# Kernel tuning notes

Measured on AMD Instinct MI355X. Metric: run time of the kernel, lower is better.

## Reference

```python
import jax, jax.numpy as jnp
import numpy as np
import math

# dims
B, L, D = 2, 2048, 1024          # batch, seq len, embedding_dim
HID, ATT, H = 1024, 512, 8       # linear_hidden_dim, attention_dim, num_heads
DQK, DUV = ATT // H, HID // H    # 64, 128
NBUCK = 64                       # time_num_buckets
MAX_SPAN = 86400 * 90            # max_time_span
EPS = 1e-6
OUT_DIM = 2 * HID + 2 * ATT      # uvqk output dim = 3072


def _time_boundaries():
    # RelativeAttentionBiasModule._build_boundaries: pure log buckets
    steps = NBUCK - 1
    log_part = np.exp(np.linspace(0.0, math.log(MAX_SPAN), steps))
    b = np.unique(np.floor(np.clip(log_part, 1, None)).astype(np.int64)).astype(np.float32)
    return jnp.asarray(b)

_BOUNDARIES = _time_boundaries()  # len <= 63, indices < NBUCK


def setup_inputs() -> dict:
    key = jax.random.key(0)
    ks = jax.random.split(key, 8)
    x = jax.random.normal(ks[0], (B, L, D), dtype=jnp.float32)
    timestamps = jnp.sort(
        jax.random.randint(ks[1], (B, L), 0, 2592000), axis=-1
    )  # chronological event times (seconds)
    attn_mask = jnp.tril(jnp.ones((L, L), dtype=bool))[None].repeat(B, axis=0)  # causal
    W_uvqk = jax.random.normal(ks[2], (OUT_DIM, D), dtype=jnp.float32) * 0.02
    b_uvqk = jnp.zeros((OUT_DIM,), dtype=jnp.float32)
    time_bias = jax.random.normal(ks[3], (NBUCK, H), dtype=jnp.float32) * 0.02
    W_o = jax.random.normal(ks[4], (D, HID), dtype=jnp.float32) * 0.02
    b_o = jnp.zeros((D,), dtype=jnp.float32)
    rms_w = jnp.ones((HID,), dtype=jnp.float32)
    return {"x": x, "timestamps": timestamps, "attn_mask": attn_mask,
            "W_uvqk": W_uvqk, "b_uvqk": b_uvqk, "time_bias": time_bias,
            "W_o": W_o, "b_o": b_o, "rms_w": rms_w}


def reference(x, timestamps, attn_mask, W_uvqk, b_uvqk, time_bias, W_o, b_o, rms_w):
    Bx, Lx, _ = x.shape
    scale = 1.0 / math.sqrt(DQK)

    # fused uvqk projection + act1 (silu)
    h = jax.nn.silu(x @ W_uvqk.T + b_uvqk)  # [B, L, OUT_DIM]
    u, v, q, k = jnp.split(h, [HID, 2 * HID, 2 * HID + ATT], axis=-1)

    def heads(t, d):  # [B, L, H*d] -> [B, H, L, d]
        return t.reshape(Bx, Lx, H, d).transpose(0, 2, 1, 3)

    u = heads(u, DUV)
    v = heads(v, DUV)
    q = heads(q, DQK) * scale
    k = heads(k, DQK)

    logits = jnp.einsum('bhid,bhjd->bhij', q.astype(jnp.float32), k.astype(jnp.float32))

    # bucketized relative-time bias (per-head)
    tdiff = jnp.abs(timestamps[:, :, None] - timestamps[:, None, :])
    tdiff = jnp.clip(tdiff, 1, None).astype(jnp.float32)  # clamp_min(1)
    bk = jnp.searchsorted(_BOUNDARIES, tdiff, side='left')  # torch.bucketize right=False
    rab = time_bias[bk].transpose(0, 3, 1, 2)  # [B, H, L, L]

    # pointwise silu attention (no softmax), masked
    A = jax.nn.silu(logits + rab) * attn_mask[:, None].astype(jnp.float32)

    y = jnp.einsum('bhij,bhjd->bhid', A, v)               # [B, H, L, DUV]
    y = y.transpose(0, 2, 1, 3).reshape(Bx, Lx, HID)       # merge heads
    u_m = u.transpose(0, 2, 1, 3).reshape(Bx, Lx, HID)

    # RMSNorm then U-gate
    rms = y * jax.lax.rsqrt(jnp.mean(y * y, axis=-1, keepdims=True) + EPS) * rms_w
    y_point = rms.astype(x.dtype) * u_m

    return y_point @ W_o.T + b_o  # [B, L, D]
```

## Files before the change

kernel.cpp:

```cpp
#include <hip/hip_runtime.h>
#include <hip/hip_bf16.h>

typedef float f32x4 __attribute__((ext_vector_type(4)));
typedef short s16x8 __attribute__((ext_vector_type(8)));
typedef short s16x4 __attribute__((ext_vector_type(4)));
typedef unsigned short u16x4 __attribute__((ext_vector_type(4)));

__device__ __forceinline__ float bf2f(unsigned short u) {
    union { unsigned int i; float f; } x; x.i = ((unsigned int)u) << 16; return x.f;
}
__device__ __forceinline__ unsigned short f2bf(float f) {
    union { float f; unsigned int i; } x; x.f = f;
    unsigned int r = x.i + 0x7FFFu + ((x.i >> 16) & 1u);
    return (unsigned short)(r >> 16);
}
__device__ __forceinline__ float silu(float v) {
    return v / (1.f + __expf(-v));
}
__device__ __forceinline__ float silu_fast(float v) {
    return v * __builtin_amdgcn_rcpf(1.f + __expf(-v));
}

#define GLDS16(gp, lp) __builtin_amdgcn_global_load_lds( \
    (const __attribute__((address_space(1))) unsigned int*)(gp), \
    (__attribute__((address_space(3))) unsigned int*)(lp), 16, 0, 0)

__global__ __launch_bounds__(256) void cvt_bf16(
    const float* __restrict__ X, const float* __restrict__ W,
    const float* __restrict__ Wo,
    unsigned short* __restrict__ Xb, unsigned short* __restrict__ Wb,
    unsigned short* __restrict__ Wob)
{
    int idx = blockIdx.x * 256 + threadIdx.x;
    const float* src; unsigned short* dst; int off;
    if (idx < 1048576)       { src = X;  dst = Xb;  off = idx; }
    else if (idx < 1835008)  { src = W;  dst = Wb;  off = idx - 1048576; }
    else                     { src = Wo; dst = Wob; off = idx - 1835008; }
    f32x4 v = *reinterpret_cast<const f32x4*>(&src[(size_t)off * 4]);
    u16x4 o;
    #pragma unroll
    for (int j = 0; j < 4; ++j) o[j] = f2bf(v[j]);
    *reinterpret_cast<u16x4*>(&dst[(size_t)off * 4]) = o;
}

__global__ __launch_bounds__(256) void bucketize(
    const int* __restrict__ TS, unsigned char* __restrict__ BK)
{
    const int jt = blockIdx.x, it = blockIdx.y, b = blockIdx.z;
    if (jt > it) return;
    __shared__ int bndRaw[63];
    __shared__ int bnd[64];
    __shared__ int tsi[64], tsj[64];
    const int tid = threadIdx.x;
    if (tid < 63) {
        double step = log(7776000.0) / 62.0;
        double v = exp(step * (double)tid);
        if (v < 1.0) v = 1.0;
        bndRaw[tid] = (int)floor(v);
    }
    if (tid >= 64 && tid < 128) tsi[tid - 64] = TS[b * 2048 + it * 64 + (tid - 64)];
    else if (tid >= 128 && tid < 192) tsj[tid - 128] = TS[b * 2048 + jt * 64 + (tid - 128)];
    __syncthreads();
    if (tid == 0) {
        int c = 0, p = -1;
        for (int i = 0; i < 63; ++i) { int x = bndRaw[i]; if (x != p) { bnd[c++] = x; p = x; } }
        for (; c < 64; ++c) bnd[c] = 0x7FFFFFFF;
    }
    __syncthreads();
    const int il = tid & 63, jc = (tid >> 6) * 16;
    const int tiv = tsi[il];
    unsigned char out[16];
    #pragma unroll
    for (int u = 0; u < 16; ++u) {
        int td = tiv - tsj[jc + u]; td = td < 0 ? -td : td; if (td < 1) td = 1;
        int pos = 0;
        #pragma unroll
        for (int st = 32; st; st >>= 1)
            if (bnd[pos + st - 1] < td) pos += st;
        out[u] = (unsigned char)pos;
    }
    *reinterpret_cast<int4*>(&BK[((size_t)b << 22) + (size_t)(it * 64 + il) * 2048 + jt * 64 + jc]) =
        *reinterpret_cast<const int4*>(out);
}

__global__ __launch_bounds__(256) void gemm_uvqk(
    const unsigned short* __restrict__ Xb, const unsigned short* __restrict__ Wb,
    const float* __restrict__ bias,
    unsigned short* __restrict__ U, unsigned short* __restrict__ Vt,
    unsigned short* __restrict__ Q, unsigned short* __restrict__ K)
{
    __shared__ __align__(16) unsigned short smem[2][128][64];
    const int tid = threadIdx.x;
    const int wv = tid >> 6, lane = tid & 63;
    const int g = lane >> 4, lr = lane & 15;
    const int wid = (blockIdx.x & 7) * 96 + (blockIdx.x >> 3);
    const int m0 = (wid & 31) * 128, n0 = (wid >> 5) * 128;
    const int wr = (wv >> 1) * 64, wc = (wv & 1) * 64;
    const int ls = lr & 7;
    f32x4 acc[4][4] = {};

    for (int k0 = 0; k0 < 1024; k0 += 64) {
        #pragma unroll
        for (int c = 0; c < 4; ++c) {
            int id = c * 256 + tid;
            int row = id >> 3, c8 = id & 7;
            int sc = (c8 ^ (row & 7)) * 8;
            GLDS16(&Xb[(size_t)(m0 + row) * 1024 + k0 + sc], &smem[0][row][c8 * 8]);
            GLDS16(&Wb[(size_t)(n0 + row) * 1024 + k0 + sc], &smem[1][row][c8 * 8]);
        }
        __syncthreads();
        s16x8 afr[4][2], bfr[4][2];
        #pragma unroll
        for (int i = 0; i < 4; ++i)
            #pragma unroll
            for (int kq = 0; kq < 2; ++kq) {
                afr[i][kq] = *reinterpret_cast<const s16x8*>(
                    &smem[0][wr + i * 16 + lr][((kq * 4 + g) ^ ls) * 8]);
                bfr[i][kq] = *reinterpret_cast<const s16x8*>(
                    &smem[1][wc + i * 16 + lr][((kq * 4 + g) ^ ls) * 8]);
            }
        #pragma unroll
        for (int kq = 0; kq < 2; ++kq)
            #pragma unroll
            for (int mi = 0; mi < 4; ++mi)
                #pragma unroll
                for (int ni = 0; ni < 4; ++ni)
                    acc[mi][ni] = __builtin_amdgcn_mfma_f32_16x16x32_bf16(
                        afr[mi][kq], bfr[ni][kq], acc[mi][ni], 0, 0, 0);
        __syncthreads();
    }

    if (n0 >= 1024 && n0 < 2048) {
        const int head = (n0 - 1024) >> 7;
        unsigned short* sT = &smem[0][0][0] + wv * (32 * 72);
        #pragma unroll
        for (int hh = 0; hh < 2; ++hh) {
            #pragma unroll
            for (int nn = 0; nn < 2; ++nn) {
                int ni = hh * 2 + nn;
                float bn = bias[n0 + wc + ni * 16 + lr];
                #pragma unroll
                for (int mi = 0; mi < 4; ++mi)
                    #pragma unroll
                    for (int r = 0; r < 4; ++r)
                        sT[(nn * 16 + lr) * 72 + mi * 16 + g * 4 + r] =
                            f2bf(silu(acc[mi][ni][r] + bn));
            }
            #pragma unroll
            for (int c = 0; c < 4; ++c) {
                int id = c * 64 + lane;
                int row = id >> 3, ch = id & 7;
                s16x8 val = *reinterpret_cast<const s16x8*>(&sT[row * 72 + ch * 8]);
                int d = wc + hh * 32 + row;
                int mg = m0 + wr + ch * 8;
                int bb = mg >> 11, l = mg & 2047;
                *reinterpret_cast<s16x8*>(
                    &Vt[(((size_t)(bb * 8 + head) * 128 + d) << 11) + l]) = val;
            }
        }
    } else {
        #pragma unroll
        for (int ni = 0; ni < 4; ++ni) {
            int n = n0 + wc + ni * 16 + lr;
            float bn = bias[n];
            #pragma unroll
            for (int mi = 0; mi < 4; ++mi) {
                #pragma unroll
                for (int r = 0; r < 4; ++r) {
                    int m = m0 + wr + mi * 16 + g * 4 + r;
                    float v = silu(acc[mi][ni][r] + bn);
                    int b = m >> 11, l = m & 2047;
                    if (n < 1024) {
                        U[(size_t)m * 1024 + n] = f2bf(v);
                    } else if (n < 2560) {
                        int dd = n - 2048, h = dd >> 6, d = dd & 63;
                        Q[((((size_t)(b * 8 + h) << 11) + l) << 6) + d] = f2bf(v * 0.125f);
                    } else {
                        int dd = n - 2560, h = dd >> 6, d = dd & 63;
                        K[((((size_t)(b * 8 + h) << 11) + l) << 6) + d] = f2bf(v);
                    }
                }
            }
        }
    }
}

__global__ __launch_bounds__(512, 1) void attn(
    const unsigned short* __restrict__ Q, const unsigned short* __restrict__ K,
    const unsigned short* __restrict__ Vt, const unsigned char* __restrict__ BK,
    const float* __restrict__ TB, float* __restrict__ Y)
{
    __shared__ __align__(16) unsigned short sK[2][2][64][64];
    __shared__ __align__(16) unsigned short sV[2][2][128][64];
    __shared__ __align__(16) unsigned char  sBK[2][2][64][64];

    const int tid = threadIdx.x, wv = tid >> 6, lane = tid & 63;
    const int g = lane >> 4, lr = lane & 15;

    const int bid = blockIdx.x;
    const int xcd = bid & 7, kix = bid >> 3;
    const int bh = 2 * xcd + (kix & 1);
    const int ti = 31 - (kix >> 1);
    const int b = bh >> 3, h = bh & 7;
    const int i0 = ti * 64;
    const int rg = wv & 3;
    const int half = wv >> 2;
    const int irow = i0 + rg * 16;
    const int P = (ti + 2) >> 1;

    const int tbl = __float_as_int(TB[lane * 8 + h]);

    const unsigned short* qb = Q + ((size_t)bh << 11) * 64;
    const unsigned short* kb = K + ((size_t)bh << 11) * 64;
    const unsigned short* vtb = Vt + ((size_t)bh << 7) * 2048;
    const unsigned char* bkb = BK + ((size_t)b << 22);

    s16x8 aq[2];
    #pragma unroll
    for (int kq = 0; kq < 2; ++kq)
        aq[kq] = *reinterpret_cast<const s16x8*>(&qb[(size_t)(irow + lr) * 64 + kq * 32 + g * 8]);

    char* sKb = (char*)&sK[0][0][0][0];
    char* sVb = (char*)&sV[0][0][0][0];
    char* sBKb = (char*)&sBK[0][0][0][0];
    const int cs = lr & 7;
    const int ib = irow + lr;

    auto stage = [&](int q, int db) {
        int jth = 2 * q + half;
        if (jth > ti) jth = 2 * q;
        const size_t j0 = (size_t)jth * 64;
        char* kd = sKb + db * 16384 + half * 8192;
        char* vd = sVb + db * 32768 + half * 16384;
        char* bkd = sBKb + db * 8192 + half * 4096;
        #pragma unroll
        for (int c = 0; c < 2; ++c) {
            int chunk = rg * 128 + c * 64 + lane;
            int row = chunk >> 3, c8 = chunk & 7;
            GLDS16(kb + (j0 + row) * 64 + ((c8 ^ (row & 7)) * 8), kd + chunk * 16);
        }
        #pragma unroll
        for (int c = 0; c < 4; ++c) {
            int chunk = rg * 256 + c * 64 + lane;
            int d = chunk >> 3, c8 = chunk & 7;
            GLDS16(vtb + (size_t)d * 2048 + j0 + ((c8 ^ (d & 7)) * 8), vd + chunk * 16);
        }
        {
            int chunk = rg * 64 + lane;
            int row = chunk >> 2, c16 = chunk & 3;
            GLDS16(bkb + (size_t)(i0 + row) * 2048 + j0 + ((c16 ^ (row & 3)) * 16), bkd + chunk * 16);
        }
    };

    f32x4 accy[8] = {};

#define COMPUTE(DB) { \
        const int jt = 2 * p + half; \
        if (jt <= ti) { \
            const char* kbase = sKb + (DB) * 16384 + half * 8192; \
            f32x4 sacc[4] = {}; \
            _Pragma("unroll") \
            for (int ni = 0; ni < 4; ++ni) { \
                _Pragma("unroll") \
                for (int kq = 0; kq < 2; ++kq) { \
                    s16x8 kf = *reinterpret_cast<const s16x8*>( \
                        kbase + (ni * 16 + lr) * 128 + (((kq * 4 + g) ^ cs) << 4)); \
                    sacc[ni] = __builtin_amdgcn_mfma_f32_16x16x32_bf16(kf, aq[kq], sacc[ni], 0, 0, 0); \
                } \
            } \
            const int j0 = jt * 64; \
            const bool diag = (jt == ti); \
            s16x4 pf[4]; \
            _Pragma("unroll") \
            for (int ni = 0; ni < 4; ++ni) { \
                unsigned int bw = *reinterpret_cast<const unsigned int*>( \
                    sBKb + (DB) * 8192 + half * 4096 + (rg * 16 + lr) * 64 + ((ni ^ (lr & 3)) << 4) + g * 4); \
                float b0 = __int_as_float(__builtin_amdgcn_ds_bpermute((int)((bw & 255u) << 2), tbl)); \
                float b1 = __int_as_float(__builtin_amdgcn_ds_bpermute((int)(((bw >> 8) & 255u) << 2), tbl)); \
                float b2 = __int_as_float(__builtin_amdgcn_ds_bpermute((int)(((bw >> 16) & 255u) << 2), tbl)); \
                float b3 = __int_as_float(__builtin_amdgcn_ds_bpermute((int)((bw >> 24) << 2), tbl)); \
                float v0 = silu_fast(sacc[ni][0] + b0); \
                float v1 = silu_fast(sacc[ni][1] + b1); \
                float v2 = silu_fast(sacc[ni][2] + b2); \
                float v3 = silu_fast(sacc[ni][3] + b3); \
                if (diag) { \
                    int jb = j0 + ni * 16 + g * 4; \
                    if (jb + 0 > ib) v0 = 0.f; \
                    if (jb + 1 > ib) v1 = 0.f; \
                    if (jb + 2 > ib) v2 = 0.f; \
                    if (jb + 3 > ib) v3 = 0.f; \
                } \
                unsigned int w0, w1; \
                asm("v_cvt_pk_bf16_f32 %0, %1, %2" : "=v"(w0) : "v"(v0), "v"(v1)); \
                asm("v_cvt_pk_bf16_f32 %0, %1, %2" : "=v"(w1) : "v"(v2), "v"(v3)); \
                union { unsigned int u_[2]; s16x4 v_; } cvt_; \
                cvt_.u_[0] = w0; cvt_.u_[1] = w1; \
                pf[ni] = cvt_.v_; \
            } \
            const char* vbase = sVb + (DB) * 32768 + half * 16384; \
            _Pragma("unroll") \
            for (int di = 0; di < 8; ++di) { \
                _Pragma("unroll") \
                for (int ni = 0; ni < 4; ++ni) { \
                    s16x4 vf = *reinterpret_cast<const s16x4*>( \
                        vbase + (di * 16 + lr) * 128 + (((2 * ni + (g >> 1)) ^ cs) << 4) + ((g & 1) << 3)); \
                    accy[di] = __builtin_amdgcn_mfma_f32_16x16x16bf16_1k(pf[ni], vf, accy[di], 0, 0, 0); \
                } \
            } \
        } }

    stage(0, 0);

    int p = 0;
    for (;;) {
        __builtin_amdgcn_s_barrier();
        if (p + 1 < P) {
            stage(p + 1, 1);
            asm volatile("s_waitcnt vmcnt(7)" ::: "memory");
        } else {
            asm volatile("s_waitcnt vmcnt(0)" ::: "memory");
        }
        __builtin_amdgcn_s_barrier();
        COMPUTE(0);
        if (++p == P) break;
        __builtin_amdgcn_s_barrier();
        if (p + 1 < P) {
            stage(p + 1, 0);
            asm volatile("s_waitcnt vmcnt(7)" ::: "memory");
        } else {
            asm volatile("s_waitcnt vmcnt(0)" ::: "memory");
        }
        __builtin_amdgcn_s_barrier();
        COMPUTE(1);
        if (++p == P) break;
    }
#undef COMPUTE

    __syncthreads();
    float* red = (float*)sVb;
    if (wv >= 4) {
        #pragma unroll
        for (int di = 0; di < 8; ++di)
            #pragma unroll
            for (int r = 0; r < 4; ++r)
                red[(rg * 16 + g * 4 + r) * 132 + di * 16 + lr] = accy[di][r];
    }
    __syncthreads();
    if (wv < 4) {
        #pragma unroll
        for (int di = 0; di < 8; ++di)
            #pragma unroll
            for (int r = 0; r < 4; ++r) {
                float s = accy[di][r] + red[(rg * 16 + g * 4 + r) * 132 + di * 16 + lr];
                Y[(size_t)((b << 11) + irow + g * 4 + r) * 1024 + h * 128 + di * 16 + lr] = s;
            }
    }
}

__global__ __launch_bounds__(256) void rmsnorm_gate(
    const float* __restrict__ Y, const unsigned short* __restrict__ U,
    const float* __restrict__ rw, unsigned short* __restrict__ YP)
{
    __shared__ float red[4];
    const int row = blockIdx.x, tid = threadIdx.x;
    f32x4 v = *reinterpret_cast<const f32x4*>(&Y[(size_t)row * 1024 + tid * 4]);
    float ss = v[0] * v[0] + v[1] * v[1] + v[2] * v[2] + v[3] * v[3];
    #pragma unroll
    for (int off = 32; off; off >>= 1) ss += __shfl_down(ss, off);
    if ((tid & 63) == 0) red[tid >> 6] = ss;
    __syncthreads();
    float rms = rsqrtf((red[0] + red[1] + red[2] + red[3]) * (1.f / 1024.f) + 1e-6f);
    #pragma unroll
    for (int j = 0; j < 4; ++j) {
        int c = tid * 4 + j;
        float o = v[j] * rms * rw[c] * bf2f(U[(size_t)row * 1024 + c]);
        YP[(size_t)row * 1024 + c] = f2bf(o);
    }
}

__global__ __launch_bounds__(512) void gemm_out(
    const unsigned short* __restrict__ YP, const unsigned short* __restrict__ Wob,
    const float* __restrict__ bo, float* __restrict__ OUT)
{
    __shared__ __align__(16) unsigned short sA[128][64];
    __shared__ __align__(16) unsigned short sB[128][64];
    const int tid = threadIdx.x;
    const int wv = tid >> 6, lane = tid & 63;
    const int g = lane >> 4, lr = lane & 15;
    const int wid = (blockIdx.x & 7) * 32 + (blockIdx.x >> 3);
    const int m0 = (wid & 31) * 128, n0 = (wid >> 5) * 128;
    const int wr = (wv >> 2) * 64, wc = (wv & 3) * 32;
    const int ls = lr & 7;
    f32x4 acc[4][2] = {};

    for (int k0 = 0; k0 < 1024; k0 += 64) {
        #pragma unroll
        for (int c = 0; c < 2; ++c) {
            int id = c * 512 + tid;
            int row = id >> 3, c8 = id & 7;
            int sc = (c8 ^ (row & 7)) * 8;
            GLDS16(&YP[(size_t)(m0 + row) * 1024 + k0 + sc], &sA[row][c8 * 8]);
            GLDS16(&Wob[(size_t)(n0 + row) * 1024 + k0 + sc], &sB[row][c8 * 8]);
        }
        __syncthreads();
        s16x8 afr[4][2], bfr[2][2];
        #pragma unroll
        for (int kq = 0; kq < 2; ++kq) {
            #pragma unroll
            for (int i = 0; i < 4; ++i)
                afr[i][kq] = *reinterpret_cast<const s16x8*>(
                    &sA[wr + i * 16 + lr][((kq * 4 + g) ^ ls) * 8]);
            #pragma unroll
            for (int i = 0; i < 2; ++i)
                bfr[i][kq] = *reinterpret_cast<const s16x8*>(
                    &sB[wc + i * 16 + lr][((kq * 4 + g) ^ ls) * 8]);
        }
        #pragma unroll
        for (int kq = 0; kq < 2; ++kq)
            #pragma unroll
            for (int mi = 0; mi < 4; ++mi)
                #pragma unroll
                for (int ni = 0; ni < 2; ++ni)
                    acc[mi][ni] = __builtin_amdgcn_mfma_f32_16x16x32_bf16(
                        afr[mi][kq], bfr[ni][kq], acc[mi][ni], 0, 0, 0);
        __syncthreads();
    }

    #pragma unroll
    for (int ni = 0; ni < 2; ++ni) {
        int n = n0 + wc + ni * 16 + lr;
        float bn = bo[n];
        #pragma unroll
        for (int mi = 0; mi < 4; ++mi)
            #pragma unroll
            for (int r = 0; r < 4; ++r) {
                int m = m0 + wr + mi * 16 + g * 4 + r;
                OUT[(size_t)m * 1024 + n] = acc[mi][ni][r] + bn;
            }
    }
}

extern "C" void kernel_launch(void* const* d_in, const int* in_sizes, int n_in,
                              void* d_out, int out_size, void* d_ws, size_t ws_size,
                              hipStream_t stream) {
    const float* X     = (const float*)d_in[0];
    const int*   TS    = (const int*)d_in[1];
    const float* Wuvqk = (const float*)d_in[3];
    const float* buvqk = (const float*)d_in[4];
    const float* TB    = (const float*)d_in[5];
    const float* Wo    = (const float*)d_in[6];
    const float* bo    = (const float*)d_in[7];
    const float* rw    = (const float*)d_in[8];
    float* OUT = (float*)d_out;

    char* ws = (char*)d_ws;
    unsigned short* Qb  = (unsigned short*)(ws);
    unsigned short* Kb  = (unsigned short*)(ws + (4u << 20));
    unsigned short* Vt  = (unsigned short*)(ws + (8u << 20));
    unsigned short* Ub  = (unsigned short*)(ws + (16u << 20));
    float*          Yb  = (float*)(ws + (24u << 20));
    unsigned short* Xb  = (unsigned short*)(ws + (24u << 20));
    unsigned short* Wb  = (unsigned short*)(ws + (32u << 20));
    unsigned short* YP  = (unsigned short*)(ws + (40u << 20));
    unsigned char*  BKm = (unsigned char*)(ws + (48u << 20));
    unsigned short* Wob = (unsigned short*)(ws + (56u << 20));

    cvt_bf16<<<8192, 256, 0, stream>>>(X, Wuvqk, Wo, Xb, Wb, Wob);
    bucketize<<<dim3(32, 32, 2), 256, 0, stream>>>(TS, BKm);
    gemm_uvqk<<<768, 256, 0, stream>>>(Xb, Wb, buvqk, Ub, Vt, Qb, Kb);
    attn<<<512, 512, 0, stream>>>(Qb, Kb, Vt, BKm, TB, Yb);
    rmsnorm_gate<<<4096, 256, 0, stream>>>(Yb, Ub, rw, YP);
    gemm_out<<<256, 512, 0, stream>>>(YP, Wob, bo, OUT);
}
```

Before: 149.7 us.

## Merge convert and bucketize kernels, store attention output in bf16, tweak GEMM loops

Fuses the bf16 conversion and time-bucketize kernels into one launch to remove a kernel launch. Stores the attention output as bf16 instead of fp32, which halves the traffic into the RMSNorm kernel at the cost of some precision before normalization. Also switches the SiLU epilogue to a reciprocal-based fast variant and restructures the GEMM inner loops to load fragments per k-step, which reduces register pressure.

New measurement: 144.6 us. 3.4% less time.

```diff
diff --git a/kernel.cpp b/kernel.cpp
--- a/kernel.cpp
+++ b/kernel.cpp
@@ -14,9 +14,6 @@
     unsigned int r = x.i + 0x7FFFu + ((x.i >> 16) & 1u);
     return (unsigned short)(r >> 16);
 }
-__device__ __forceinline__ float silu(float v) {
-    return v / (1.f + __expf(-v));
-}
 __device__ __forceinline__ float silu_fast(float v) {
     return v * __builtin_amdgcn_rcpf(1.f + __expf(-v));
 }
@@ -25,33 +22,32 @@
     (const __attribute__((address_space(1))) unsigned int*)(gp), \
     (__attribute__((address_space(3))) unsigned int*)(lp), 16, 0, 0)
 
-__global__ __launch_bounds__(256) void cvt_bf16(
+__global__ __launch_bounds__(256) void cvt_bucketize(
     const float* __restrict__ X, const float* __restrict__ W,
-    const float* __restrict__ Wo,
+    const float* __restrict__ Wo, const int* __restrict__ TS,
     unsigned short* __restrict__ Xb, unsigned short* __restrict__ Wb,
-    unsigned short* __restrict__ Wob)
+    unsigned short* __restrict__ Wob, unsigned char* __restrict__ BK)
 {
-    int idx = blockIdx.x * 256 + threadIdx.x;
-    const float* src; unsigned short* dst; int off;
-    if (idx < 1048576)       { src = X;  dst = Xb;  off = idx; }
-    else if (idx < 1835008)  { src = W;  dst = Wb;  off = idx - 1048576; }
-    else                     { src = Wo; dst = Wob; off = idx - 1835008; }
-    f32x4 v = *reinterpret_cast<const f32x4*>(&src[(size_t)off * 4]);
-    u16x4 o;
-    #pragma unroll
-    for (int j = 0; j < 4; ++j) o[j] = f2bf(v[j]);
-    *reinterpret_cast<u16x4*>(&dst[(size_t)off * 4]) = o;
-}
-
-__global__ __launch_bounds__(256) void bucketize(
-    const int* __restrict__ TS, unsigned char* __restrict__ BK)
-{
-    const int jt = blockIdx.x, it = blockIdx.y, b = blockIdx.z;
+    const int tid = threadIdx.x;
+    if (blockIdx.x < 8192) {
+        int idx = blockIdx.x * 256 + tid;
+        const float* src; unsigned short* dst; int off;
+        if (idx < 1048576)       { src = X;  dst = Xb;  off = idx; }
+        else if (idx < 1835008)  { src = W;  dst = Wb;  off = idx - 1048576; }
+        else                     { src = Wo; dst = Wob; off = idx - 1835008; }
+        f32x4 v = *reinterpret_cast<const f32x4*>(&src[(size_t)off * 4]);
+        u16x4 o;
+        #pragma unroll
+        for (int j = 0; j < 4; ++j) o[j] = f2bf(v[j]);
+        *reinterpret_cast<u16x4*>(&dst[(size_t)off * 4]) = o;
+        return;
+    }
+    const int bid = blockIdx.x - 8192;
+    const int jt = bid & 31, it = (bid >> 5) & 31, b = bid >> 10;
     if (jt > it) return;
     __shared__ int bndRaw[63];
     __shared__ int bnd[64];
     __shared__ int tsi[64], tsj[64];
-    const int tid = threadIdx.x;
     if (tid < 63) {
         double step = log(7776000.0) / 62.0;
         double v = exp(step * (double)tid);
@@ -89,7 +85,8 @@
     unsigned short* __restrict__ U, unsigned short* __restrict__ Vt,
     unsigned short* __restrict__ Q, unsigned short* __restrict__ K)
 {
-    __shared__ __align__(16) unsigned short smem[2][128][64];
+    __shared__ __align__(16) unsigned short sA[128][64];
+    __shared__ __align__(16) unsigned short sB[128][64];
     const int tid = threadIdx.x;
     const int wv = tid >> 6, lane = tid & 63;
     const int g = lane >> 4, lr = lane & 15;
@@ -105,34 +102,33 @@
             int id = c * 256 + tid;
             int row = id >> 3, c8 = id & 7;
             int sc = (c8 ^ (row & 7)) * 8;
-            GLDS16(&Xb[(size_t)(m0 + row) * 1024 + k0 + sc], &smem[0][row][c8 * 8]);
-            GLDS16(&Wb[(size_t)(n0 + row) * 1024 + k0 + sc], &smem[1][row][c8 * 8]);
+            GLDS16(&Xb[(size_t)(m0 + row) * 1024 + k0 + sc], &sA[row][c8 * 8]);
+            GLDS16(&Wb[(size_t)(n0 + row) * 1024 + k0 + sc], &sB[row][c8 * 8]);
         }
         __syncthreads();
-        s16x8 afr[4][2], bfr[4][2];
-        #pragma unroll
-        for (int i = 0; i < 4; ++i)
-            #pragma unroll
-            for (int kq = 0; kq < 2; ++kq) {
-                afr[i][kq] = *reinterpret_cast<const s16x8*>(
-                    &smem[0][wr + i * 16 + lr][((kq * 4 + g) ^ ls) * 8]);
-                bfr[i][kq] = *reinterpret_cast<const s16x8*>(
-                    &smem[1][wc + i * 16 + lr][((kq * 4 + g) ^ ls) * 8]);
-            }
-        #pragma unroll
-        for (int kq = 0; kq < 2; ++kq)
+        #pragma unroll
+        for (int kq = 0; kq < 2; ++kq) {
+            s16x8 afr[4], bfr[4];
+            #pragma unroll
+            for (int i = 0; i < 4; ++i) {
+                afr[i] = *reinterpret_cast<const s16x8*>(
+                    &sA[wr + i * 16 + lr][((kq * 4 + g) ^ ls) * 8]);
+                bfr[i] = *reinterpret_cast<const s16x8*>(
+                    &sB[wc + i * 16 + lr][((kq * 4 + g) ^ ls) * 8]);
+            }
             #pragma unroll
             for (int mi = 0; mi < 4; ++mi)
                 #pragma unroll
                 for (int ni = 0; ni < 4; ++ni)
                     acc[mi][ni] = __builtin_amdgcn_mfma_f32_16x16x32_bf16(
-                        afr[mi][kq], bfr[ni][kq], acc[mi][ni], 0, 0, 0);
+                        afr[mi], bfr[ni], acc[mi][ni], 0, 0, 0);
+        }
         __syncthreads();
     }
 
     if (n0 >= 1024 && n0 < 2048) {
         const int head = (n0 - 1024) >> 7;
-        unsigned short* sT = &smem[0][0][0] + wv * (32 * 72);
+        unsigned short* sT = &sA[0][0] + wv * (32 * 72);
         #pragma unroll
         for (int hh = 0; hh < 2; ++hh) {
             #pragma unroll
@@ -144,7 +140,7 @@
                     #pragma unroll
                     for (int r = 0; r < 4; ++r)
                         sT[(nn * 16 + lr) * 72 + mi * 16 + g * 4 + r] =
-                            f2bf(silu(acc[mi][ni][r] + bn));
+                            f2bf(silu_fast(acc[mi][ni][r] + bn));
             }
             #pragma unroll
             for (int c = 0; c < 4; ++c) {
@@ -168,7 +164,7 @@
                 #pragma unroll
                 for (int r = 0; r < 4; ++r) {
                     int m = m0 + wr + mi * 16 + g * 4 + r;
-                    float v = silu(acc[mi][ni][r] + bn);
+                    float v = silu_fast(acc[mi][ni][r] + bn);
                     int b = m >> 11, l = m & 2047;
                     if (n < 1024) {
                         U[(size_t)m * 1024 + n] = f2bf(v);
@@ -188,7 +184,7 @@
 __global__ __launch_bounds__(512, 1) void attn(
     const unsigned short* __restrict__ Q, const unsigned short* __restrict__ K,
     const unsigned short* __restrict__ Vt, const unsigned char* __restrict__ BK,
-    const float* __restrict__ TB, float* __restrict__ Y)
+    const float* __restrict__ TB, unsigned short* __restrict__ Y)
 {
     __shared__ __align__(16) unsigned short sK[2][2][64][64];
     __shared__ __align__(16) unsigned short sV[2][2][128][64];
@@ -352,18 +348,21 @@
             #pragma unroll
             for (int r = 0; r < 4; ++r) {
                 float s = accy[di][r] + red[(rg * 16 + g * 4 + r) * 132 + di * 16 + lr];
-                Y[(size_t)((b << 11) + irow + g * 4 + r) * 1024 + h * 128 + di * 16 + lr] = s;
+                Y[(size_t)((b << 11) + irow + g * 4 + r) * 1024 + h * 128 + di * 16 + lr] = f2bf(s);
             }
     }
 }
 
 __global__ __launch_bounds__(256) void rmsnorm_gate(
-    const float* __restrict__ Y, const unsigned short* __restrict__ U,
+    const unsigned short* __restrict__ Y, const unsigned short* __restrict__ U,
     const float* __restrict__ rw, unsigned short* __restrict__ YP)
 {
     __shared__ float red[4];
     const int row = blockIdx.x, tid = threadIdx.x;
-    f32x4 v = *reinterpret_cast<const f32x4*>(&Y[(size_t)row * 1024 + tid * 4]);
+    u16x4 v4 = *reinterpret_cast<const u16x4*>(&Y[(size_t)row * 1024 + tid * 4]);
+    float v[4];
+    #pragma unroll
+    for (int j = 0; j < 4; ++j) v[j] = bf2f(v4[j]);
     float ss = v[0] * v[0] + v[1] * v[1] + v[2] * v[2] + v[3] * v[3];
     #pragma unroll
     for (int off = 32; off; off >>= 1) ss += __shfl_down(ss, off);
@@ -403,26 +402,24 @@
             GLDS16(&Wob[(size_t)(n0 + row) * 1024 + k0 + sc], &sB[row][c8 * 8]);
         }
         __syncthreads();
-        s16x8 afr[4][2], bfr[2][2];
         #pragma unroll
         for (int kq = 0; kq < 2; ++kq) {
+            s16x8 afr[4], bfr[2];
             #pragma unroll
             for (int i = 0; i < 4; ++i)
-                afr[i][kq] = *reinterpret_cast<const s16x8*>(
+                afr[i] = *reinterpret_cast<const s16x8*>(
                     &sA[wr + i * 16 + lr][((kq * 4 + g) ^ ls) * 8]);
             #pragma unroll
             for (int i = 0; i < 2; ++i)
-                bfr[i][kq] = *reinterpret_cast<const s16x8*>(
+                bfr[i] = *reinterpret_cast<const s16x8*>(
                     &sB[wc + i * 16 + lr][((kq * 4 + g) ^ ls) * 8]);
-        }
-        #pragma unroll
-        for (int kq = 0; kq < 2; ++kq)
             #pragma unroll
             for (int mi = 0; mi < 4; ++mi)
                 #pragma unroll
                 for (int ni = 0; ni < 2; ++ni)
                     acc[mi][ni] = __builtin_amdgcn_mfma_f32_16x16x32_bf16(
-                        afr[mi][kq], bfr[ni][kq], acc[mi][ni], 0, 0, 0);
+                        afr[mi], bfr[ni], acc[mi][ni], 0, 0, 0);
+        }
         __syncthreads();
     }
 
@@ -458,15 +455,14 @@
     unsigned short* Kb  = (unsigned short*)(ws + (4u << 20));
     unsigned short* Vt  = (unsigned short*)(ws + (8u << 20));
     unsigned short* Ub  = (unsigned short*)(ws + (16u << 20));
-    float*          Yb  = (float*)(ws + (24u << 20));
+    unsigned short* Yb  = (unsigned short*)(ws + (24u << 20));
     unsigned short* Xb  = (unsigned short*)(ws + (24u << 20));
     unsigned short* Wb  = (unsigned short*)(ws + (32u << 20));
     unsigned short* YP  = (unsigned short*)(ws + (40u << 20));
     unsigned char*  BKm = (unsigned char*)(ws + (48u << 20));
     unsigned short* Wob = (unsigned short*)(ws + (56u << 20));
 
-    cvt_bf16<<<8192, 256, 0, stream>>>(X, Wuvqk, Wo, Xb, Wb, Wob);
-    bucketize<<<dim3(32, 32, 2), 256, 0, stream>>>(TS, BKm);
+    cvt_bucketize<<<10240, 256, 0, stream>>>(X, Wuvqk, Wo, TS, Xb, Wb, Wob, BKm);
     gemm_uvqk<<<768, 256, 0, stream>>>(Xb, Wb, buvqk, Ub, Vt, Qb, Kb);
     attn<<<512, 512, 0, stream>>>(Qb, Kb, Vt, BKm, TB, Yb);
     rmsnorm_gate<<<4096, 256, 0, stream>>>(Yb, Ub, rw, YP);
```
